# Kernel optimization log

Measured on AMD Instinct MI355X. Metric: run time of the kernel, lower is better.

Reference implementation:

```python
import jax, jax.numpy as jnp
import numpy as np

N_NODES = 50000
N_EDGES = 800000
N_GRAPHS = 64
N_REL = 8
NHID = 128
HID2 = 2 * NHID  # nhid + nhid_structre = 256
N_CLASSES = 10
LN_EPS = 1e-5
NEG_SLOPE = 0.01


def rgcn(x, src, dst, etype, W, root, bias):
    # PyG RGCNConv: per-relation linear transform, mean-aggregate per (dst, relation),
    # sum over relations, plus root transform and bias.
    N = x.shape[0]
    R = W.shape[0]
    xW = jnp.einsum('nc,rcd->rnd', x, W)          # [R, N, out]
    msg = xW[etype, src]                           # [E, out] gather per edge
    idx = dst * R + etype                          # combined (node, relation) segment id
    ones = jnp.ones(etype.shape[0], x.dtype)
    cnt = jax.ops.segment_sum(ones, idx, num_segments=N * R).reshape(N, R)
    norm = 1.0 / jnp.maximum(cnt[dst, etype], 1.0)  # 1/deg_r(dst) -> mean aggregation
    agg = jax.ops.segment_sum(msg * norm[:, None], dst, num_segments=N)
    return agg + x @ root + bias


def gap(x, batch, num_graphs):
    s = jax.ops.segment_sum(x, batch, num_segments=num_graphs)
    c = jax.ops.segment_sum(jnp.ones(x.shape[0], x.dtype), batch, num_segments=num_graphs)
    return s / jnp.maximum(c, 1.0)[:, None]


def layer_norm(x, g, b):
    m = x.mean(-1, keepdims=True)
    v = ((x - m) ** 2).mean(-1, keepdims=True)
    return (x - m) / jnp.sqrt(v + LN_EPS) * g + b


def mha1(x, in_w, in_b, out_w, out_b):
    # nn.MultiheadAttention, num_heads=1, x: [L, N, E] (seq-first)
    E = x.shape[-1]
    qkv = x @ in_w.T + in_b
    q, k, v = jnp.split(qkv, 3, axis=-1)
    scores = jnp.einsum('lne,mne->nlm', q, k) / jnp.sqrt(jnp.asarray(E, x.dtype))
    a = jax.nn.softmax(scores, axis=-1)
    o = jnp.einsum('nlm,mne->lne', a, v)
    return o @ out_w.T + out_b


def setup_inputs() -> dict:
    key = jax.random.key(0)
    ks = list(jax.random.split(key, 24))
    f32 = jnp.float32
    p = lambda k, shape, fan: jax.random.normal(k, shape, f32) / np.sqrt(fan)
    inp = {}
    inp['x'] = jax.random.normal(ks[0], (N_NODES, NHID), f32)
    inp['edge_index'] = jax.random.randint(ks[1], (2, N_EDGES), 0, N_NODES, jnp.int32)
    inp['edge_attr'] = jax.random.randint(ks[2], (N_EDGES,), 0, N_REL, jnp.int32)
    inp['batch'] = jnp.sort(jax.random.randint(ks[3], (N_NODES,), 0, N_GRAPHS, jnp.int32))
    # structure_rgcn1..3 : 128 -> 128 (stacked)
    inp['Ws'] = p(ks[4], (3, N_REL, NHID, NHID), NHID)
    inp['Rs'] = p(ks[5], (3, NHID, NHID), NHID)
    inp['Bs'] = jnp.zeros((3, NHID), f32)
    # feature_rgcn : 128 -> 128
    inp['Wf1'] = p(ks[6], (N_REL, NHID, NHID), NHID)
    inp['Rf1'] = p(ks[7], (NHID, NHID), NHID)
    inp['Bf1'] = jnp.zeros((NHID,), f32)
    # feature_rgcn2/3 : 256 -> 128 (stacked)
    inp['Wf23'] = p(ks[8], (2, N_REL, HID2, NHID), HID2)
    inp['Rf23'] = p(ks[9], (2, HID2, NHID), HID2)
    inp['Bf23'] = jnp.zeros((2, NHID), f32)
    # feature_rgcn4 : 256 -> 256
    inp['Wf4'] = p(ks[10], (N_REL, HID2, HID2), HID2)
    inp['Rf4'] = p(ks[11], (HID2, HID2), HID2)
    inp['Bf4'] = jnp.zeros((HID2,), f32)
    # transformer encoder (single head)
    inp['attn_in_w'] = p(ks[12], (3 * HID2, HID2), HID2)
    inp['attn_in_b'] = jnp.zeros((3 * HID2,), f32)
    inp['attn_out_w'] = p(ks[13], (HID2, HID2), HID2)
    inp['attn_out_b'] = jnp.zeros((HID2,), f32)
    inp['enc_fc_w'] = p(ks[14], (HID2, HID2), HID2)
    inp['enc_fc_b'] = jnp.zeros((HID2,), f32)
    inp['enc_ln_g'] = jnp.ones((HID2,), f32)
    inp['enc_ln_b'] = jnp.zeros((HID2,), f32)
    # final classifier
    inp['out_w'] = p(ks[15], (N_CLASSES, HID2), HID2)
    inp['out_b'] = jnp.zeros((N_CLASSES,), f32)
    return inp


def reference(x, edge_index, edge_attr, batch, Ws, Rs, Bs, Wf1, Rf1, Bf1,
              Wf23, Rf23, Bf23, Wf4, Rf4, Bf4, attn_in_w, attn_in_b,
              attn_out_w, attn_out_b, enc_fc_w, enc_fc_b, enc_ln_g, enc_ln_b,
              out_w, out_b):
    act = lambda t: jax.nn.leaky_relu(t, NEG_SLOPE)
    src, dst = edge_index[0], edge_index[1]
    # structure lane
    x1 = act(rgcn(x, src, dst, edge_attr, Ws[0], Rs[0], Bs[0]))
    x2 = act(rgcn(x1, src, dst, edge_attr, Ws[1], Rs[1], Bs[1]))
    x3 = act(rgcn(x2, src, dst, edge_attr, Ws[2], Rs[2], Bs[2]))
    se1 = gap(x1, batch, N_GRAPHS)[batch] + x1
    se2 = gap(x2, batch, N_GRAPHS)[batch] + x2
    se3 = gap(x3, batch, N_GRAPHS)[batch] + x3
    # feature lane
    h = act(rgcn(x, src, dst, edge_attr, Wf1, Rf1, Bf1))
    h = jnp.concatenate([h, se1], axis=-1)
    h = act(rgcn(h, src, dst, edge_attr, Wf23[0], Rf23[0], Bf23[0]))
    h = jnp.concatenate([h, se2], axis=-1)
    h = act(rgcn(h, src, dst, edge_attr, Wf23[1], Rf23[1], Bf23[1]))
    q = jnp.concatenate([h, se3], axis=-1)
    q = act(rgcn(q, src, dst, edge_attr, Wf4, Rf4, Bf4))  # fixed: rgcn4 on concat (dim 2*nhid)
    # transformer encoder over [L=1, N, 2*nhid] (eval mode, dropout off)
    Q = q[None, :, :]
    a = mha1(Q, attn_in_w, attn_in_b, attn_out_w, attn_out_b)
    a = layer_norm(a + Q, enc_ln_g, enc_ln_b)
    f = a @ enc_fc_w.T + enc_fc_b
    o = layer_norm(f + a, enc_ln_g, enc_ln_b)  # same LN params reused, as in source
    pooled = gap(o[0], batch, N_GRAPHS)
    return pooled @ out_w.T + out_b
```

## Files before the change

### kernel.cpp

```cpp
#include <hip/hip_runtime.h>
#include <cstdint>
#include <cstddef>

#define NREL 8
#define NG 64
#define LN_EPS 1e-5f
#define NEG_SLOPE 0.01f

typedef unsigned short u16;
typedef short bf16x8 __attribute__((ext_vector_type(8)));
typedef float f32x4 __attribute__((ext_vector_type(4)));

static __device__ __forceinline__ float b2f(u16 h) {
  return __uint_as_float(((unsigned)h) << 16);
}
static __device__ __forceinline__ u16 f2b(float f) {
  unsigned u = __float_as_uint(f);
  u += 0x7fffu + ((u >> 16) & 1u);
  return (u16)(u >> 16);
}
static __device__ __forceinline__ void upadd8(uint4 v, float* a) {
  a[0] += b2f((u16)(v.x & 0xffff)); a[1] += b2f((u16)(v.x >> 16));
  a[2] += b2f((u16)(v.y & 0xffff)); a[3] += b2f((u16)(v.y >> 16));
  a[4] += b2f((u16)(v.z & 0xffff)); a[5] += b2f((u16)(v.z >> 16));
  a[6] += b2f((u16)(v.w & 0xffff)); a[7] += b2f((u16)(v.w >> 16));
}
static __device__ __forceinline__ uint4 pack8(const float* a) {
  uint4 o;
  o.x = (unsigned)f2b(a[0]) | ((unsigned)f2b(a[1]) << 16);
  o.y = (unsigned)f2b(a[2]) | ((unsigned)f2b(a[3]) << 16);
  o.z = (unsigned)f2b(a[4]) | ((unsigned)f2b(a[5]) << 16);
  o.w = (unsigned)f2b(a[6]) | ((unsigned)f2b(a[7]) << 16);
  return o;
}

__global__ void count_edges_k(const int* __restrict__ dst, const int* __restrict__ et,
                              int* __restrict__ cnt, int E) {
  int e = blockIdx.x * blockDim.x + threadIdx.x;
  if (e < E) atomicAdd(&cnt[dst[e] * NREL + et[e]], 1);
}

__global__ void graph_inv_k(const int* __restrict__ batch, float* __restrict__ ginv, int N) {
  int g = threadIdx.x;
  if (g >= NG) return;
  int a, b;
  { int l = 0, h = N; while (l < h) { int m = (l + h) >> 1; if (batch[m] < g) l = m + 1; else h = m; } a = l; }
  { int l = 0, h = N; while (l < h) { int m = (l + h) >> 1; if (batch[m] < g + 1) l = m + 1; else h = m; } b = l; }
  ginv[g] = 1.0f / fmaxf((float)(b - a), 1.0f);
}

#define SCAN_B 256
#define SCAN_I 4

__global__ void scan1_k(const int* __restrict__ in, int* __restrict__ out,
                        int* __restrict__ bsum, int n) {
  __shared__ int sh[SCAN_B];
  int b0 = blockIdx.x * (SCAN_B * SCAN_I);
  int t = threadIdx.x;
  int v[SCAN_I]; int s = 0;
#pragma unroll
  for (int i = 0; i < SCAN_I; ++i) {
    int idx = b0 + t * SCAN_I + i;
    v[i] = idx < n ? in[idx] : 0;
    s += v[i];
  }
  sh[t] = s; __syncthreads();
  for (int off = 1; off < SCAN_B; off <<= 1) {
    int x = (t >= off) ? sh[t - off] : 0; __syncthreads();
    sh[t] += x; __syncthreads();
  }
  int excl = sh[t] - s;
  if (t == SCAN_B - 1) bsum[blockIdx.x] = sh[t];
  int run = excl;
#pragma unroll
  for (int i = 0; i < SCAN_I; ++i) {
    int idx = b0 + t * SCAN_I + i;
    if (idx < n) out[idx] = run;
    run += v[i];
  }
}

__global__ void scan2_k(int* __restrict__ bsum, int nb) {
  __shared__ int sh[1024];
  int t = threadIdx.x;
  int v = t < nb ? bsum[t] : 0;
  sh[t] = v; __syncthreads();
  for (int off = 1; off < 1024; off <<= 1) {
    int x = (t >= off) ? sh[t - off] : 0; __syncthreads();
    sh[t] += x; __syncthreads();
  }
  if (t < nb) bsum[t] = sh[t] - v;
}

__global__ void scan3_k(int* __restrict__ out, const int* __restrict__ bsum, int n, int total) {
  int idx = blockIdx.x * blockDim.x + threadIdx.x;
  if (idx < n) out[idx] += bsum[idx / (SCAN_B * SCAN_I)];
  if (idx == 0) out[n] = total;
}

__global__ void scatter_k(const int* __restrict__ src, const int* __restrict__ dst,
                          const int* __restrict__ et, const int* __restrict__ batch,
                          int* __restrict__ cursor, int* __restrict__ srcs,
                          int* __restrict__ bsrc, int E) {
  int e = blockIdx.x * blockDim.x + threadIdx.x;
  if (e >= E) return;
  int s = src[e];
  int key = dst[e] * NREL + et[e];
  int p = atomicAdd(&cursor[key], 1);
  srcs[p] = s;
  bsrc[p] = batch[s];
}

__global__ void wtrans_k(const float* __restrict__ in, u16* __restrict__ out,
                         int rstride, int coff, int D, int ldout) {
  __shared__ float tl[32][33];
  int c0 = blockIdx.x * 32;
  int d0 = blockIdx.y * 32;
  int t = threadIdx.x;
  int r = c0 >> 7;
  int rowbase = r * rstride + (c0 & 127) + coff;
#pragma unroll
  for (int i = 0; i < 4; ++i) {
    int cl = (t >> 5) + i * 8;
    tl[cl][t & 31] = in[(size_t)(rowbase + cl) * D + d0 + (t & 31)];
  }
  __syncthreads();
#pragma unroll
  for (int i = 0; i < 4; ++i) {
    int dl = (t >> 5) + i * 8;
    out[(size_t)(d0 + dl) * ldout + c0 + (t & 31)] = f2b(tl[t & 31][dl]);
  }
}

__global__ void wcfold_k(const float* __restrict__ wo, const float* __restrict__ wv,
                         const float* __restrict__ bv, const float* __restrict__ bo,
                         u16* __restrict__ wc, float* __restrict__ bc) {
  __shared__ float worow[256];
  int n = blockIdx.x, j = threadIdx.x;
  worow[j] = wo[n * 256 + j];
  __syncthreads();
  float s = 0.f;
#pragma unroll 4
  for (int m = 0; m < 256; ++m) s += worow[m] * wv[(size_t)m * 256 + j];
  wc[(size_t)n * 256 + j] = f2b(s);
  if (j == 0) {
    float b = bo[n];
    for (int m = 0; m < 256; ++m) b += worow[m] * bv[m];
    bc[n] = b;
  }
}

__global__ void castf_k(const float* __restrict__ in, u16* __restrict__ out, int n) {
  int i = (blockIdx.x * blockDim.x + threadIdx.x) * 4;
  if (i >= n) return;
  float4 v = *(const float4*)(in + i);
  ushort4 o;
  o.x = f2b(v.x); o.y = f2b(v.y); o.z = f2b(v.z); o.w = f2b(v.w);
  *(ushort4*)(out + i) = o;
}

__global__ void agg_csr_b(const int* __restrict__ srcs, const int* __restrict__ off,
                          const u16* __restrict__ xin, int xstride,
                          u16* __restrict__ S, int NSEG) {
  int gid = blockIdx.x * blockDim.x + threadIdx.x;
  int seg = gid >> 4;
  int lane = gid & 15;
  if (seg >= NSEG) return;
  int a = off[seg], b = off[seg + 1];
  float inv = 1.0f / fmaxf((float)(b - a), 1.0f);
  float ac[8] = {0.f, 0.f, 0.f, 0.f, 0.f, 0.f, 0.f, 0.f};
  for (int e = a; e < b; ++e) {
    uint4 v = *(const uint4*)(xin + (size_t)srcs[e] * xstride + lane * 8);
    upadd8(v, ac);
  }
#pragma unroll
  for (int i = 0; i < 8; ++i) ac[i] *= inv;
  *(uint4*)(S + (size_t)seg * 128 + lane * 8) = pack8(ac);
}

template<int WN, bool ACC, int ACTMODE>
__global__ __launch_bounds__(WN * 128)
void gemm_pool(const u16* __restrict__ Sa, int Kagg,
               const u16* __restrict__ dir0, int ds0,
               const u16* __restrict__ dir1, int ds1,
               const u16* __restrict__ Bp, int ldb,
               const float* __restrict__ bias, u16* __restrict__ C,
               int M, int N, int Ktot) {
  constexpr int BN = WN * 64;
  constexpr int CPT = 64 / WN;
  constexpr int SLOTS = CPT / 8;
  __shared__ u16 As[128 * 64];
  __shared__ u16 Bs[BN * 64];
  int bm = blockIdx.x * 128;
  int bn = blockIdx.y * BN;
  int t = threadIdx.x;
  int lane = t & 63;
  int wid = t >> 6;
  int wm = (wid / WN) * 64, wn = (wid % WN) * 64;
  int l15 = lane & 15, l4 = lane >> 4;

  f32x4 acc[4][4];
#pragma unroll
  for (int i = 0; i < 4; ++i)
#pragma unroll
    for (int j = 0; j < 4; ++j)
      acc[i][j] = (f32x4){0.f, 0.f, 0.f, 0.f};

  int srow = t / WN, sub = t % WN;
  int arow = bm + srow;
  int swz = srow & 7;
  int srB = t >> 1;
  int sB32 = (t & 1) * 32;
  int swzB = srB & 7;
  const u16* bpp = Bp + (size_t)(bn + srB) * ldb + sB32;

  for (int k0 = 0; k0 < Ktot; k0 += 64) {
    __syncthreads();
    {
      const u16* ap;
      if (k0 < Kagg) {
        ap = Sa + (size_t)arow * Kagg + k0;
      } else {
        int kd = k0 - Kagg;
        ap = (kd & 128) ? (dir1 + (size_t)arow * ds1 + (kd & 127))
                        : (dir0 + (size_t)arow * ds0 + (kd & 127));
      }
      ap += sub * CPT;
#pragma unroll
      for (int s = 0; s < SLOTS; ++s) {
        uint4 v = make_uint4(0, 0, 0, 0);
        if (arow < M) v = *(const uint4*)(ap + s * 8);
        int slot = (sub * SLOTS + s) ^ swz;
        *(uint4*)&As[srow * 64 + slot * 8] = v;
      }
    }
#pragma unroll
    for (int i = 0; i < 4; ++i) {
      uint4 v = *(const uint4*)(bpp + k0 + i * 8);
      *(uint4*)&Bs[srB * 64 + ((((t & 1) * 4 + i) ^ swzB) << 3)] = v;
    }
    __syncthreads();

#pragma unroll
    for (int kk = 0; kk < 2; ++kk) {
      bf16x8 aF[4], bF[4];
#pragma unroll
      for (int mi = 0; mi < 4; ++mi) {
        int row = wm + mi * 16 + l15;
        int slot = (kk * 4 + l4) ^ (row & 7);
        aF[mi] = *(const bf16x8*)&As[row * 64 + slot * 8];
      }
#pragma unroll
      for (int ni = 0; ni < 4; ++ni) {
        int row = wn + ni * 16 + l15;
        int slot = (kk * 4 + l4) ^ (row & 7);
        bF[ni] = *(const bf16x8*)&Bs[row * 64 + slot * 8];
      }
#pragma unroll
      for (int mi = 0; mi < 4; ++mi)
#pragma unroll
        for (int ni = 0; ni < 4; ++ni)
          acc[mi][ni] = __builtin_amdgcn_mfma_f32_16x16x32_bf16(
              bF[ni], aF[mi], acc[mi][ni], 0, 0, 0);
    }
  }

#pragma unroll
  for (int mi = 0; mi < 4; ++mi) {
    int m = bm + wm + mi * 16 + l15;
    if (m >= M) continue;
#pragma unroll
    for (int ni = 0; ni < 4; ++ni) {
      int nb = bn + wn + ni * 16 + l4 * 4;
      float v0 = acc[mi][ni][0], v1 = acc[mi][ni][1];
      float v2 = acc[mi][ni][2], v3 = acc[mi][ni][3];
      u16* cp = C + (size_t)m * N + nb;
      if (ACC) {
        ushort4 o = *(const ushort4*)cp;
        v0 += b2f(o.x); v1 += b2f(o.y); v2 += b2f(o.z); v3 += b2f(o.w);
      } else {
        float4 bv = *(const float4*)(bias + nb);
        v0 += bv.x; v1 += bv.y; v2 += bv.z; v3 += bv.w;
      }
      bool da = (ACTMODE == 1) || (ACTMODE == 2 && !(nb & 128));
      if (da) {
        v0 = v0 > 0.f ? v0 : NEG_SLOPE * v0;
        v1 = v1 > 0.f ? v1 : NEG_SLOPE * v1;
        v2 = v2 > 0.f ? v2 : NEG_SLOPE * v2;
        v3 = v3 > 0.f ? v3 : NEG_SLOPE * v3;
      }
      ushort4 o;
      o.x = f2b(v0); o.y = f2b(v1); o.z = f2b(v2); o.w = f2b(v3);
      *(ushort4*)cp = o;
    }
  }
}

__global__ __launch_bounds__(512)
void gemm_ln(const u16* __restrict__ A, const u16* __restrict__ Bp,
             const float* __restrict__ bias, const u16* __restrict__ res,
             const float* __restrict__ gp, const float* __restrict__ bpar,
             u16* __restrict__ out, int M) {
  __shared__ u16 As[128 * 64];
  __shared__ u16 Bs[256 * 64];
  __shared__ float2 part[4][128];
  int bm = blockIdx.x * 128;
  int t = threadIdx.x;
  int lane = t & 63;
  int wid = t >> 6;
  int wm = (wid >> 2) * 64, wn = (wid & 3) * 64;
  int l15 = lane & 15, l4 = lane >> 4;

  f32x4 acc[4][4];
#pragma unroll
  for (int i = 0; i < 4; ++i)
#pragma unroll
    for (int j = 0; j < 4; ++j)
      acc[i][j] = (f32x4){0.f, 0.f, 0.f, 0.f};

  int srow = t >> 2, sub = t & 3;
  int arow = bm + srow;
  int swz = srow & 7;
  int srB = t >> 1;
  int sB32 = (t & 1) * 32;
  int swzB = srB & 7;
  const u16* bpp = Bp + (size_t)srB * 256 + sB32;

  for (int k0 = 0; k0 < 256; k0 += 64) {
    __syncthreads();
    {
      const u16* ap = A + (size_t)arow * 256 + k0 + sub * 16;
#pragma unroll
      for (int s = 0; s < 2; ++s) {
        uint4 v = make_uint4(0, 0, 0, 0);
        if (arow < M) v = *(const uint4*)(ap + s * 8);
        int slot = (sub * 2 + s) ^ swz;
        *(uint4*)&As[srow * 64 + slot * 8] = v;
      }
    }
#pragma unroll
    for (int i = 0; i < 4; ++i) {
      uint4 v = *(const uint4*)(bpp + k0 + i * 8);
      *(uint4*)&Bs[srB * 64 + ((((t & 1) * 4 + i) ^ swzB) << 3)] = v;
    }
    __syncthreads();

#pragma unroll
    for (int kk = 0; kk < 2; ++kk) {
      bf16x8 aF[4], bF[4];
#pragma unroll
      for (int mi = 0; mi < 4; ++mi) {
        int row = wm + mi * 16 + l15;
        int slot = (kk * 4 + l4) ^ (row & 7);
        aF[mi] = *(const bf16x8*)&As[row * 64 + slot * 8];
      }
#pragma unroll
      for (int ni = 0; ni < 4; ++ni) {
        int row = wn + ni * 16 + l15;
        int slot = (kk * 4 + l4) ^ (row & 7);
        bF[ni] = *(const bf16x8*)&Bs[row * 64 + slot * 8];
      }
#pragma unroll
      for (int mi = 0; mi < 4; ++mi)
#pragma unroll
        for (int ni = 0; ni < 4; ++ni)
          acc[mi][ni] = __builtin_amdgcn_mfma_f32_16x16x32_bf16(
              bF[ni], aF[mi], acc[mi][ni], 0, 0, 0);
    }
  }

#pragma unroll
  for (int mi = 0; mi < 4; ++mi) {
    int m = bm + wm + mi * 16 + l15;
    float s = 0.f, q = 0.f;
#pragma unroll
    for (int ni = 0; ni < 4; ++ni) {
      int nb = wn + ni * 16 + l4 * 4;
      float4 bv = *(const float4*)(bias + nb);
      ushort4 rv = make_ushort4(0, 0, 0, 0);
      if (m < M) rv = *(const ushort4*)(res + (size_t)m * 256 + nb);
      float y0 = acc[mi][ni][0] + bv.x + b2f(rv.x);
      float y1 = acc[mi][ni][1] + bv.y + b2f(rv.y);
      float y2 = acc[mi][ni][2] + bv.z + b2f(rv.z);
      float y3 = acc[mi][ni][3] + bv.w + b2f(rv.w);
      acc[mi][ni] = (f32x4){y0, y1, y2, y3};
      s += y0 + y1 + y2 + y3;
      q += y0 * y0 + y1 * y1 + y2 * y2 + y3 * y3;
    }
    s += __shfl_xor(s, 16); s += __shfl_xor(s, 32);
    q += __shfl_xor(q, 16); q += __shfl_xor(q, 32);
    if (l4 == 0) part[wid & 3][wm + mi * 16 + l15] = make_float2(s, q);
  }
  __syncthreads();
#pragma unroll
  for (int mi = 0; mi < 4; ++mi) {
    int row = wm + mi * 16 + l15;
    int m = bm + row;
    float S = 0.f, Q = 0.f;
#pragma unroll
    for (int c = 0; c < 4; ++c) {
      float2 pp = part[c][row];
      S += pp.x; Q += pp.y;
    }
    float mean = S * (1.0f / 256.0f);
    float var = fmaxf(Q * (1.0f / 256.0f) - mean * mean, 0.f);
    float rinv = rsqrtf(var + LN_EPS);
    if (m >= M) continue;
#pragma unroll
    for (int ni = 0; ni < 4; ++ni) {
      int nb = wn + ni * 16 + l4 * 4;
      float4 vg = *(const float4*)(gp + nb);
      float4 vb = *(const float4*)(bpar + nb);
      ushort4 o;
      o.x = f2b((acc[mi][ni][0] - mean) * rinv * vg.x + vb.x);
      o.y = f2b((acc[mi][ni][1] - mean) * rinv * vg.y + vb.y);
      o.z = f2b((acc[mi][ni][2] - mean) * rinv * vg.z + vb.z);
      o.w = f2b((acc[mi][ni][3] - mean) * rinv * vg.w + vb.w);
      *(ushort4*)(out + (size_t)m * 256 + nb) = o;
    }
  }
}

__global__ void gap_sum_b(const u16* __restrict__ x, int xstride,
                          const int* __restrict__ batch,
                          float* __restrict__ out, int N, int C, int npb) {
  int d = threadIdx.x;
  int n0 = blockIdx.x * npb;
  if (n0 >= N) return;
  int n1 = min(n0 + npb, N);
  float acc = 0.f;
  int g = batch[n0];
  for (int n = n0; n < n1; ++n) {
    int gn = batch[n];
    if (gn != g) { atomicAdd(&out[g * C + d], acc); acc = 0.f; g = gn; }
    acc += b2f(x[(size_t)n * xstride + d]);
  }
  atomicAdd(&out[g * C + d], acc);
}

__global__ void hcalc_k(const float* __restrict__ gapb, const float* __restrict__ ginv,
                        const u16* __restrict__ Wp, int ldw,
                        const u16* __restrict__ Rp, int ldr,
                        float* __restrict__ H, float* __restrict__ T, int D) {
  __shared__ float G[128];
  int g = blockIdx.x;
  int t = threadIdx.x;
  G[t] = gapb[g * 128 + t] * ginv[g];
  __syncthreads();
  int d = blockIdx.y * 128 + t;
#pragma unroll 1
  for (int r = 0; r < 8; ++r) {
    float s = 0.f;
    const u16* wp = Wp + (size_t)d * ldw + r * 128;
#pragma unroll 4
    for (int c = 0; c < 128; ++c) s += G[c] * b2f(wp[c]);
    H[((size_t)g * 8 + r) * D + d] = s;
  }
  float s = 0.f;
  const u16* rp = Rp + (size_t)d * ldr;
#pragma unroll 4
  for (int c = 0; c < 128; ++c) s += G[c] * b2f(rp[c]);
  T[(size_t)g * D + d] = s;
}

template<int D>
__global__ void finish_k(u16* __restrict__ out, int ldo,
                         const u16* __restrict__ m, int ldm,
                         const float* __restrict__ H, const float* __restrict__ T,
                         const int* __restrict__ off, const int* __restrict__ bsrc,
                         const int* __restrict__ batch, int N) {
  const int L = D / 4;
  const int NPB = 256 / L;
  int t = threadIdx.x;
  int n = blockIdx.x * NPB + t / L;
  if (n >= N) return;
  int l = t % L;
  int cols = l * 4;
  ushort4 o = *(const ushort4*)(out + (size_t)n * ldo + cols);
  float v0 = b2f(o.x), v1 = b2f(o.y), v2 = b2f(o.z), v3 = b2f(o.w);
  if (m) {
    ushort4 mm = *(const ushort4*)(m + (size_t)n * ldm + cols);
    v0 += b2f(mm.x); v1 += b2f(mm.y); v2 += b2f(mm.z); v3 += b2f(mm.w);
  }
  float4 tv = *(const float4*)(T + (size_t)batch[n] * D + cols);
  v0 += tv.x; v1 += tv.y; v2 += tv.z; v3 += tv.w;
#pragma unroll 1
  for (int r = 0; r < 8; ++r) {
    int a = off[n * 8 + r], b = off[n * 8 + r + 1];
    if (a == b) continue;
    float inv = 1.0f / (float)(b - a);
    float h0 = 0.f, h1 = 0.f, h2 = 0.f, h3 = 0.f;
    for (int e = a; e < b; ++e) {
      float4 hv = *(const float4*)(H + ((size_t)bsrc[e] * 8 + r) * D + cols);
      h0 += hv.x; h1 += hv.y; h2 += hv.z; h3 += hv.w;
    }
    v0 += inv * h0; v1 += inv * h1; v2 += inv * h2; v3 += inv * h3;
  }
  v0 = v0 > 0.f ? v0 : NEG_SLOPE * v0;
  v1 = v1 > 0.f ? v1 : NEG_SLOPE * v1;
  v2 = v2 > 0.f ? v2 : NEG_SLOPE * v2;
  v3 = v3 > 0.f ? v3 : NEG_SLOPE * v3;
  ushort4 w;
  w.x = f2b(v0); w.y = f2b(v1); w.z = f2b(v2); w.w = f2b(v3);
  *(ushort4*)(out + (size_t)n * ldo + cols) = w;
}

__global__ void head_k(const float* __restrict__ psum, const float* __restrict__ ginv,
                       const float* __restrict__ ow, const float* __restrict__ ob,
                       float* __restrict__ out) {
  int gr = blockIdx.x;
  int lane = threadIdx.x;
  float gi = ginv[gr];
  float4 v = *(const float4*)(psum + gr * 256 + lane * 4);
  float p0 = v.x * gi, p1 = v.y * gi, p2 = v.z * gi, p3 = v.w * gi;
  for (int cls = 0; cls < 10; ++cls) {
    float4 w = *(const float4*)(ow + cls * 256 + lane * 4);
    float s = p0 * w.x + p1 * w.y + p2 * w.z + p3 * w.w;
#pragma unroll
    for (int o = 32; o > 0; o >>= 1) s += __shfl_xor(s, o);
    if (lane == 0) out[gr * 10 + cls] = s + ob[cls];
  }
}

extern "C" void kernel_launch(void* const* d_in, const int* in_sizes, int n_in,
                              void* d_out, int out_size, void* d_ws, size_t ws_size,
                              hipStream_t stream) {
  const float* x        = (const float*)d_in[0];
  const int*   eidx     = (const int*)d_in[1];
  const int*   eattr    = (const int*)d_in[2];
  const int*   batch    = (const int*)d_in[3];
  const float* Ws       = (const float*)d_in[4];
  const float* Rs       = (const float*)d_in[5];
  const float* Bsb      = (const float*)d_in[6];
  const float* Wf1      = (const float*)d_in[7];
  const float* Rf1      = (const float*)d_in[8];
  const float* Bf1      = (const float*)d_in[9];
  const float* Wf23     = (const float*)d_in[10];
  const float* Rf23     = (const float*)d_in[11];
  const float* Bf23     = (const float*)d_in[12];
  const float* Wf4      = (const float*)d_in[13];
  const float* Rf4      = (const float*)d_in[14];
  const float* Bf4      = (const float*)d_in[15];
  const float* attn_in_w  = (const float*)d_in[16];
  const float* attn_in_b  = (const float*)d_in[17];
  const float* attn_out_w = (const float*)d_in[18];
  const float* attn_out_b = (const float*)d_in[19];
  const float* enc_fc_w   = (const float*)d_in[20];
  const float* enc_fc_b   = (const float*)d_in[21];
  const float* ln_g       = (const float*)d_in[22];
  const float* ln_bb      = (const float*)d_in[23];
  const float* out_w      = (const float*)d_in[24];
  const float* out_b      = (const float*)d_in[25];

  const int N = in_sizes[0] / 128;
  const int E = in_sizes[1] / 2;
  const int NK = N * NREL;
  const int* src = eidx;
  const int* dst = eidx + E;

  char* p = (char*)d_ws;
  auto alloc = [&](size_t bytes) {
    char* r = p;
    p += (bytes + 255) & ~(size_t)255;
    return r;
  };
  float* ginv  = (float*)alloc(NG * 4);
  float* psum  = (float*)alloc(NG * 256 * 4);
  float* gapb  = (float*)alloc(NG * 128 * 4);
  float* bias14 = (float*)alloc(256 * 4);
  float* bias2m = (float*)alloc(256 * 4);
  float* bias3m = (float*)alloc(256 * 4);
  float* bcomb  = (float*)alloc(256 * 4);
  float* H5 = (float*)alloc((size_t)NG * 8 * 128 * 4);
  float* T5 = (float*)alloc((size_t)NG * 128 * 4);
  float* H6 = (float*)alloc((size_t)NG * 8 * 128 * 4);
  float* T6 = (float*)alloc((size_t)NG * 128 * 4);
  float* H7 = (float*)alloc((size_t)NG * 8 * 256 * 4);
  float* T7 = (float*)alloc((size_t)NG * 256 * 4);
  u16* xb   = (u16*)alloc((size_t)N * 128 * 2);
  u16* xh14 = (u16*)alloc((size_t)N * 256 * 2);
  u16* x2m5 = (u16*)alloc((size_t)N * 256 * 2);
  u16* x3m6 = (u16*)alloc((size_t)N * 256 * 2);
  u16* h5   = (u16*)alloc((size_t)N * 128 * 2);
  u16* h6   = (u16*)alloc((size_t)N * 128 * 2);
  int* cnt    = (int*)alloc((size_t)NK * 4);
  int* off    = (int*)alloc((size_t)(NK + 1) * 4);
  int* cursor = (int*)alloc((size_t)NK * 4);
  int* srcs   = (int*)alloc((size_t)E * 4);
  int* bsrc   = (int*)alloc((size_t)E * 4);
  int* bsum   = (int*)alloc(2048 * 4);
  u16* p14 = (u16*)alloc((size_t)256 * 1152 * 2);
  u16* p2m = (u16*)alloc((size_t)256 * 1152 * 2);
  u16* p3m = (u16*)alloc((size_t)256 * 1152 * 2);
  u16* p5  = (u16*)alloc((size_t)128 * 1280 * 2);
  u16* p6  = (u16*)alloc((size_t)128 * 1280 * 2);
  u16* p7a = (u16*)alloc((size_t)256 * 1152 * 2);
  u16* p7b = (u16*)alloc((size_t)256 * 1152 * 2);
  u16* wc  = (u16*)alloc((size_t)256 * 256 * 2);
  u16* wf  = (u16*)alloc((size_t)256 * 256 * 2);
  u16* S   = (u16*)alloc((size_t)N * 1024 * 2);

  u16* qpart = xh14;
  u16* t1 = x2m5;

  auto cdiv = [](long long a, long long b) { return (int)((a + b - 1) / b); };
  int gm = cdiv(N, 128);
  dim3 g1(gm, 1);

  hipMemsetAsync(cnt, 0, (size_t)NK * 4, stream);
  count_edges_k<<<cdiv(E, 256), 256, 0, stream>>>(dst, eattr, cnt, E);
  int nb = cdiv(NK, SCAN_B * SCAN_I);
  scan1_k<<<nb, SCAN_B, 0, stream>>>(cnt, off, bsum, NK);
  scan2_k<<<1, 1024, 0, stream>>>(bsum, nb);
  scan3_k<<<cdiv(NK, 256), 256, 0, stream>>>(off, bsum, NK, E);
  hipMemcpyAsync(cursor, off, (size_t)NK * 4, hipMemcpyDeviceToDevice, stream);
  scatter_k<<<cdiv(E, 256), 256, 0, stream>>>(src, dst, eattr, batch, cursor, srcs, bsrc, E);
  graph_inv_k<<<1, 64, 0, stream>>>(batch, ginv, N);

  castf_k<<<cdiv((long long)N * 128, 1024), 256, 0, stream>>>(x, xb, N * 128);
  hipMemsetAsync(p2m, 0, (size_t)256 * 1152 * 2, stream);
  hipMemsetAsync(p3m, 0, (size_t)256 * 1152 * 2, stream);
  dim3 gw(32, 4), gwD2(32, 8), gr(4, 4), grD2(4, 8);
  const float* W6 = Wf23 + (size_t)8 * 256 * 128;
  wtrans_k<<<gw, 256, 0, stream>>>(Ws,  p14,                        128, 0, 128, 1152);
  wtrans_k<<<gr, 256, 0, stream>>>(Rs,  p14 + 1024,                 128, 0, 128, 1152);
  wtrans_k<<<gw, 256, 0, stream>>>(Wf1, p14 + (size_t)128 * 1152,        128, 0, 128, 1152);
  wtrans_k<<<gr, 256, 0, stream>>>(Rf1, p14 + (size_t)128 * 1152 + 1024, 128, 0, 128, 1152);
  wtrans_k<<<gw, 256, 0, stream>>>(Ws + (size_t)8 * 128 * 128, p2m,        128, 0, 128, 1152);
  wtrans_k<<<gr, 256, 0, stream>>>(Rs + 128 * 128,             p2m + 1024, 128, 0, 128, 1152);
  wtrans_k<<<gw, 256, 0, stream>>>(Wf23, p2m + (size_t)128 * 1152, 256, 128, 128, 1152);
  wtrans_k<<<gw, 256, 0, stream>>>(Ws + (size_t)16 * 128 * 128, p3m,        128, 0, 128, 1152);
  wtrans_k<<<gr, 256, 0, stream>>>(Rs + 2 * 128 * 128,          p3m + 1024, 128, 0, 128, 1152);
  wtrans_k<<<gw, 256, 0, stream>>>(W6, p3m + (size_t)128 * 1152, 256, 128, 128, 1152);
  wtrans_k<<<gw, 256, 0, stream>>>(Wf23, p5,        256, 0,   128, 1280);
  wtrans_k<<<gr, 256, 0, stream>>>(Rf23, p5 + 1024, 256, 0,   128, 1280);
  wtrans_k<<<gr, 256, 0, stream>>>(Rf23, p5 + 1152, 256, 128, 128, 1280);
  wtrans_k<<<gw, 256, 0, stream>>>(W6,               p6,        256, 0,   128, 1280);
  wtrans_k<<<gr, 256, 0, stream>>>(Rf23 + 256 * 128, p6 + 1024, 256, 0,   128, 1280);
  wtrans_k<<<gr, 256, 0, stream>>>(Rf23 + 256 * 128, p6 + 1152, 256, 128, 128, 1280);
  wtrans_k<<<gwD2, 256, 0, stream>>>(Wf4, p7a,        256, 0,   256, 1152);
  wtrans_k<<<grD2, 256, 0, stream>>>(Rf4, p7a + 1024, 256, 0,   256, 1152);
  wtrans_k<<<gwD2, 256, 0, stream>>>(Wf4, p7b,        256, 128, 256, 1152);
  wtrans_k<<<grD2, 256, 0, stream>>>(Rf4, p7b + 1024, 256, 128, 256, 1152);
  wcfold_k<<<256, 256, 0, stream>>>(attn_out_w, attn_in_w + (size_t)512 * 256,
                                    attn_in_b + 512, attn_out_b, wc, bcomb);
  castf_k<<<cdiv(256 * 256, 1024), 256, 0, stream>>>(enc_fc_w, wf, 256 * 256);
  hipMemcpyAsync(bias14, Bsb, 512, hipMemcpyDeviceToDevice, stream);
  hipMemcpyAsync(bias14 + 128, Bf1, 512, hipMemcpyDeviceToDevice, stream);
  hipMemsetAsync(bias2m, 0, 1024, stream);
  hipMemcpyAsync(bias2m, Bsb + 128, 512, hipMemcpyDeviceToDevice, stream);
  hipMemsetAsync(bias3m, 0, 1024, stream);
  hipMemcpyAsync(bias3m, Bsb + 256, 512, hipMemcpyDeviceToDevice, stream);

  int aggGrid = cdiv((long long)NK * 16, 256);

  agg_csr_b<<<aggGrid, 256, 0, stream>>>(srcs, off, xb, 128, S, NK);
  gemm_pool<4, false, 1><<<g1, 512, 0, stream>>>(S, 1024, xb, 128, nullptr, 0,
                                                 p14, 1152, bias14, xh14, N, 256, 1152);
  hipMemsetAsync(gapb, 0, NG * 128 * 4, stream);
  gap_sum_b<<<cdiv(N, 64), 128, 0, stream>>>(xh14, 256, batch, gapb, N, 128, 64);
  hcalc_k<<<dim3(64, 1), 128, 0, stream>>>(gapb, ginv, p2m + (size_t)128 * 1152, 1152,
                                           p5 + 1152, 1280, H5, T5, 128);
  agg_csr_b<<<aggGrid, 256, 0, stream>>>(srcs, off, xh14, 256, S, NK);
  gemm_pool<4, false, 2><<<g1, 512, 0, stream>>>(S, 1024, xh14, 256, nullptr, 0,
                                                 p2m, 1152, bias2m, x2m5, N, 256, 1152);
  hipMemsetAsync(gapb, 0, NG * 128 * 4, stream);
  gap_sum_b<<<cdiv(N, 64), 128, 0, stream>>>(x2m5, 256, batch, gapb, N, 128, 64);
  hcalc_k<<<dim3(64, 1), 128, 0, stream>>>(gapb, ginv, p3m + (size_t)128 * 1152, 1152,
                                           p6 + 1152, 1280, H6, T6, 128);

  agg_csr_b<<<aggGrid, 256, 0, stream>>>(srcs, off, x2m5, 256, S, NK);
  gemm_pool<4, false, 2><<<g1, 512, 0, stream>>>(S, 1024, x2m5, 256, nullptr, 0,
                                                 p3m, 1152, bias3m, x3m6, N, 256, 1152);
  hipMemsetAsync(gapb, 0, NG * 128 * 4, stream);
  gap_sum_b<<<cdiv(N, 64), 128, 0, stream>>>(x3m6, 256, batch, gapb, N, 128, 64);
  hcalc_k<<<dim3(64, 2), 128, 0, stream>>>(gapb, ginv, p7b, 1152,
                                           p7b + 1024, 1152, H7, T7, 256);

  agg_csr_b<<<aggGrid, 256, 0, stream>>>(srcs, off, xh14 + 128, 256, S, NK);
  gemm_pool<2, false, 0><<<g1, 256, 0, stream>>>(S, 1024, xh14 + 128, 256, xh14, 256,
                                                 p5, 1280, Bf23, h5, N, 128, 1280);
  finish_k<128><<<cdiv(N, 8), 256, 0, stream>>>(h5, 128, x2m5 + 128, 256,
                                                H5, T5, off, bsrc, batch, N);
  agg_csr_b<<<aggGrid, 256, 0, stream>>>(srcs, off, h5, 128, S, NK);
  gemm_pool<2, false, 0><<<g1, 256, 0, stream>>>(S, 1024, h5, 128, x2m5, 256,
                                                 p6, 1280, Bf23 + 128, h6, N, 128, 1280);
  finish_k<128><<<cdiv(N, 8), 256, 0, stream>>>(h6, 128, x3m6 + 128, 256,
                                                H6, T6, off, bsrc, batch, N);
  agg_csr_b<<<aggGrid, 256, 0, stream>>>(srcs, off, h6, 128, S, NK);
  gemm_pool<4, false, 0><<<g1, 512, 0, stream>>>(S, 1024, h6, 128, nullptr, 0,
                                                 p7a, 1152, Bf4, qpart, N, 256, 1152);
  agg_csr_b<<<aggGrid, 256, 0, stream>>>(srcs, off, x3m6, 256, S, NK);
  gemm_pool<4, true, 0><<<g1, 512, 0, stream>>>(S, 1024, x3m6, 256, nullptr, 0,
                                                p7b, 1152, nullptr, qpart, N, 256, 1152);
  finish_k<256><<<cdiv(N, 4), 256, 0, stream>>>(qpart, 256, nullptr, 0,
                                                H7, T7, off, bsrc, batch, N);

  gemm_ln<<<g1, 512, 0, stream>>>(qpart, wc, bcomb, qpart, ln_g, ln_bb, t1, N);
  gemm_ln<<<g1, 512, 0, stream>>>(t1, wf, enc_fc_b, t1, ln_g, ln_bb, qpart, N);

  hipMemsetAsync(psum, 0, NG * 256 * 4, stream);
  gap_sum_b<<<cdiv(N, 64), 256, 0, stream>>>(qpart, 256, batch, psum, N, 256, 64);
  head_k<<<64, 64, 0, stream>>>(psum, ginv, out_w, out_b, (float*)d_out);
}
```

Measured before the change: 1.342 ms.

## Flatten finish_k edge loop with precomputed per-edge weights; parallelize hcalc over relations

The scatter now stores a combined (graph*8+relation) index for each edge, and a new wedge_k kernel writes each edge's 1/deg weight into an int2 per edge. This lets finish_k walk one flat edge range per node, unrolled by two, instead of a serial loop over 8 relations with per-relation offsets and divides. agg_csr_b's gather loop is also unrolled by two to raise memory-level parallelism. hcalc_k gains a grid dimension over the 8 relations plus the root term, so it launches 9x more blocks. The cost is an extra preprocessing kernel and a doubled per-edge metadata buffer.

```diff
diff --git a/kernel.cpp b/kernel.cpp
--- a/kernel.cpp
+++ b/kernel.cpp
@@ -101,14 +101,24 @@
 __global__ void scatter_k(const int* __restrict__ src, const int* __restrict__ dst,
                           const int* __restrict__ et, const int* __restrict__ batch,
                           int* __restrict__ cursor, int* __restrict__ srcs,
-                          int* __restrict__ bsrc, int E) {
+                          int2* __restrict__ einfo, int E) {
   int e = blockIdx.x * blockDim.x + threadIdx.x;
   if (e >= E) return;
   int s = src[e];
-  int key = dst[e] * NREL + et[e];
+  int r = et[e];
+  int key = dst[e] * NREL + r;
   int p = atomicAdd(&cursor[key], 1);
   srcs[p] = s;
-  bsrc[p] = batch[s];
+  einfo[p].x = batch[s] * NREL + r;
+}
+
+__global__ void wedge_k(const int* __restrict__ off, int2* __restrict__ einfo, int NK) {
+  int s = blockIdx.x * blockDim.x + threadIdx.x;
+  if (s >= NK) return;
+  int a = off[s], b = off[s + 1];
+  if (a == b) return;
+  int wb = __float_as_int(1.0f / (float)(b - a));
+  for (int e = a; e < b; ++e) einfo[e].y = wb;
 }
 
 __global__ void wtrans_k(const float* __restrict__ in, u16* __restrict__ out,
@@ -169,7 +179,15 @@
   int a = off[seg], b = off[seg + 1];
   float inv = 1.0f / fmaxf((float)(b - a), 1.0f);
   float ac[8] = {0.f, 0.f, 0.f, 0.f, 0.f, 0.f, 0.f, 0.f};
-  for (int e = a; e < b; ++e) {
+  int e = a;
+  for (; e + 1 < b; e += 2) {
+    int s0 = srcs[e], s1 = srcs[e + 1];
+    uint4 v0 = *(const uint4*)(xin + (size_t)s0 * xstride + lane * 8);
+    uint4 v1 = *(const uint4*)(xin + (size_t)s1 * xstride + lane * 8);
+    upadd8(v0, ac);
+    upadd8(v1, ac);
+  }
+  if (e < b) {
     uint4 v = *(const uint4*)(xin + (size_t)srcs[e] * xstride + lane * 8);
     upadd8(v, ac);
   }
@@ -447,27 +465,28 @@
   int t = threadIdx.x;
   G[t] = gapb[g * 128 + t] * ginv[g];
   __syncthreads();
-  int d = blockIdx.y * 128 + t;
-#pragma unroll 1
-  for (int r = 0; r < 8; ++r) {
+  int ry = blockIdx.y;
+  int d = blockIdx.z * 128 + t;
+  if (ry < 8) {
+    const u16* wp = Wp + (size_t)d * ldw + ry * 128;
     float s = 0.f;
-    const u16* wp = Wp + (size_t)d * ldw + r * 128;
 #pragma unroll 4
     for (int c = 0; c < 128; ++c) s += G[c] * b2f(wp[c]);
-    H[((size_t)g * 8 + r) * D + d] = s;
-  }
-  float s = 0.f;
-  const u16* rp = Rp + (size_t)d * ldr;
+    H[((size_t)g * 8 + ry) * D + d] = s;
+  } else {
+    const u16* rp = Rp + (size_t)d * ldr;
+    float s = 0.f;
 #pragma unroll 4
-  for (int c = 0; c < 128; ++c) s += G[c] * b2f(rp[c]);
-  T[(size_t)g * D + d] = s;
+    for (int c = 0; c < 128; ++c) s += G[c] * b2f(rp[c]);
+    T[(size_t)g * D + d] = s;
+  }
 }
 
 template<int D>
 __global__ void finish_k(u16* __restrict__ out, int ldo,
                          const u16* __restrict__ m, int ldm,
                          const float* __restrict__ H, const float* __restrict__ T,
-                         const int* __restrict__ off, const int* __restrict__ bsrc,
+                         const int* __restrict__ off, const int2* __restrict__ einfo,
                          const int* __restrict__ batch, int N) {
   const int L = D / 4;
   const int NPB = 256 / L;
@@ -484,17 +503,23 @@
   }
   float4 tv = *(const float4*)(T + (size_t)batch[n] * D + cols);
   v0 += tv.x; v1 += tv.y; v2 += tv.z; v3 += tv.w;
-#pragma unroll 1
-  for (int r = 0; r < 8; ++r) {
-    int a = off[n * 8 + r], b = off[n * 8 + r + 1];
-    if (a == b) continue;
-    float inv = 1.0f / (float)(b - a);
-    float h0 = 0.f, h1 = 0.f, h2 = 0.f, h3 = 0.f;
-    for (int e = a; e < b; ++e) {
-      float4 hv = *(const float4*)(H + ((size_t)bsrc[e] * 8 + r) * D + cols);
-      h0 += hv.x; h1 += hv.y; h2 += hv.z; h3 += hv.w;
-    }
-    v0 += inv * h0; v1 += inv * h1; v2 += inv * h2; v3 += inv * h3;
+  int a = off[n * 8], b = off[n * 8 + 8];
+  int e = a;
+  for (; e + 1 < b; e += 2) {
+    int2 i0 = einfo[e], i1 = einfo[e + 1];
+    float w0 = __int_as_float(i0.y), w1 = __int_as_float(i1.y);
+    float4 h0 = *(const float4*)(H + (size_t)i0.x * D + cols);
+    float4 h1 = *(const float4*)(H + (size_t)i1.x * D + cols);
+    v0 += w0 * h0.x + w1 * h1.x;
+    v1 += w0 * h0.y + w1 * h1.y;
+    v2 += w0 * h0.z + w1 * h1.z;
+    v3 += w0 * h0.w + w1 * h1.w;
+  }
+  if (e < b) {
+    int2 i0 = einfo[e];
+    float w0 = __int_as_float(i0.y);
+    float4 h0 = *(const float4*)(H + (size_t)i0.x * D + cols);
+    v0 += w0 * h0.x; v1 += w0 * h0.y; v2 += w0 * h0.z; v3 += w0 * h0.w;
   }
   v0 = v0 > 0.f ? v0 : NEG_SLOPE * v0;
   v1 = v1 > 0.f ? v1 : NEG_SLOPE * v1;
@@ -587,7 +612,7 @@
   int* off    = (int*)alloc((size_t)(NK + 1) * 4);
   int* cursor = (int*)alloc((size_t)NK * 4);
   int* srcs   = (int*)alloc((size_t)E * 4);
-  int* bsrc   = (int*)alloc((size_t)E * 4);
+  int2* einfo = (int2*)alloc((size_t)E * 8);
   int* bsum   = (int*)alloc(2048 * 4);
   u16* p14 = (u16*)alloc((size_t)256 * 1152 * 2);
   u16* p2m = (u16*)alloc((size_t)256 * 1152 * 2);
@@ -614,7 +639,8 @@
   scan2_k<<<1, 1024, 0, stream>>>(bsum, nb);
   scan3_k<<<cdiv(NK, 256), 256, 0, stream>>>(off, bsum, NK, E);
   hipMemcpyAsync(cursor, off, (size_t)NK * 4, hipMemcpyDeviceToDevice, stream);
-  scatter_k<<<cdiv(E, 256), 256, 0, stream>>>(src, dst, eattr, batch, cursor, srcs, bsrc, E);
+  scatter_k<<<cdiv(E, 256), 256, 0, stream>>>(src, dst, eattr, batch, cursor, srcs, einfo, E);
+  wedge_k<<<cdiv(NK, 256), 256, 0, stream>>>(off, einfo, NK);
   graph_inv_k<<<1, 64, 0, stream>>>(batch, ginv, N);
 
   castf_k<<<cdiv((long long)N * 128, 1024), 256, 0, stream>>>(x, xb, N * 128);
@@ -659,34 +685,34 @@
                                                  p14, 1152, bias14, xh14, N, 256, 1152);
   hipMemsetAsync(gapb, 0, NG * 128 * 4, stream);
   gap_sum_b<<<cdiv(N, 64), 128, 0, stream>>>(xh14, 256, batch, gapb, N, 128, 64);
-  hcalc_k<<<dim3(64, 1), 128, 0, stream>>>(gapb, ginv, p2m + (size_t)128 * 1152, 1152,
-                                           p5 + 1152, 1280, H5, T5, 128);
+  hcalc_k<<<dim3(64, 9, 1), 128, 0, stream>>>(gapb, ginv, p2m + (size_t)128 * 1152, 1152,
+                                              p5 + 1152, 1280, H5, T5, 128);
   agg_csr_b<<<aggGrid, 256, 0, stream>>>(srcs, off, xh14, 256, S, NK);
   gemm_pool<4, false, 2><<<g1, 512, 0, stream>>>(S, 1024, xh14, 256, nullptr, 0,
                                                  p2m, 1152, bias2m, x2m5, N, 256, 1152);
   hipMemsetAsync(gapb, 0, NG * 128 * 4, stream);
   gap_sum_b<<<cdiv(N, 64), 128, 0, stream>>>(x2m5, 256, batch, gapb, N, 128, 64);
-  hcalc_k<<<dim3(64, 1), 128, 0, stream>>>(gapb, ginv, p3m + (size_t)128 * 1152, 1152,
-                                           p6 + 1152, 1280, H6, T6, 128);
+  hcalc_k<<<dim3(64, 9, 1), 128, 0, stream>>>(gapb, ginv, p3m + (size_t)128 * 1152, 1152,
+                                              p6 + 1152, 1280, H6, T6, 128);
 
   agg_csr_b<<<aggGrid, 256, 0, stream>>>(srcs, off, x2m5, 256, S, NK);
   gemm_pool<4, false, 2><<<g1, 512, 0, stream>>>(S, 1024, x2m5, 256, nullptr, 0,
                                                  p3m, 1152, bias3m, x3m6, N, 256, 1152);
   hipMemsetAsync(gapb, 0, NG * 128 * 4, stream);
   gap_sum_b<<<cdiv(N, 64), 128, 0, stream>>>(x3m6, 256, batch, gapb, N, 128, 64);
-  hcalc_k<<<dim3(64, 2), 128, 0, stream>>>(gapb, ginv, p7b, 1152,
-                                           p7b + 1024, 1152, H7, T7, 256);
+  hcalc_k<<<dim3(64, 9, 2), 128, 0, stream>>>(gapb, ginv, p7b, 1152,
+                                              p7b + 1024, 1152, H7, T7, 256);
 
   agg_csr_b<<<aggGrid, 256, 0, stream>>>(srcs, off, xh14 + 128, 256, S, NK);
   gemm_pool<2, false, 0><<<g1, 256, 0, stream>>>(S, 1024, xh14 + 128, 256, xh14, 256,
                                                  p5, 1280, Bf23, h5, N, 128, 1280);
   finish_k<128><<<cdiv(N, 8), 256, 0, stream>>>(h5, 128, x2m5 + 128, 256,
-                                                H5, T5, off, bsrc, batch, N);
+                                                H5, T5, off, einfo, batch, N);
   agg_csr_b<<<aggGrid, 256, 0, stream>>>(srcs, off, h5, 128, S, NK);
   gemm_pool<2, false, 0><<<g1, 256, 0, stream>>>(S, 1024, h5, 128, x2m5, 256,
                                                  p6, 1280, Bf23 + 128, h6, N, 128, 1280);
   finish_k<128><<<cdiv(N, 8), 256, 0, stream>>>(h6, 128, x3m6 + 128, 256,
-                                                H6, T6, off, bsrc, batch, N);
+                                                H6, T6, off, einfo, batch, N);
   agg_csr_b<<<aggGrid, 256, 0, stream>>>(srcs, off, h6, 128, S, NK);
   gemm_pool<4, false, 0><<<g1, 512, 0, stream>>>(S, 1024, h6, 128, nullptr, 0,
                                                  p7a, 1152, Bf4, qpart, N, 256, 1152);
@@ -694,7 +720,7 @@
   gemm_pool<4, true, 0><<<g1, 512, 0, stream>>>(S, 1024, x3m6, 256, nullptr, 0,
                                                 p7b, 1152, nullptr, qpart, N, 256, 1152);
   finish_k<256><<<cdiv(N, 4), 256, 0, stream>>>(qpart, 256, nullptr, 0,
-                                                H7, T7, off, bsrc, batch, N);
+                                                H7, T7, off, einfo, batch, N);
 
   gemm_ln<<<g1, 512, 0, stream>>>(qpart, wc, bcomb, qpart, ln_g, ln_bb, t1, N);
   gemm_ln<<<g1, 512, 0, stream>>>(t1, wf, enc_fc_b, t1, ln_g, ln_bb, qpart, N);
```

Measured after the change: 1.181 ms. 12.0% less time.
